# Kernel tuning notes

Measured on AMD Instinct MI355X. Metric: run time of the kernel, lower is better.

The kernel has to match this reference:

```python
import jax, jax.numpy as jnp
import numpy as np

B, H, P, L = 8, 512, 512, 2048
HIGH_STAB, LOW_STAB = 0.9, 0.99  # 0 <= high < |lambda| <= low <= 1 (discrete dynamics)


def setup_inputs() -> dict:
    key = jax.random.key(0)
    k_u, k_mag, k_ph, k_b, k_c, k_d = jax.random.split(key, 6)
    u = jax.random.normal(k_u, (B, H, L), dtype=jnp.float32)
    # Frozen diagonal reservoir state matrix Lambda_bar: complex eigenvalues with
    # magnitude in (high_stability, low_stability], random phase (stored as real/imag pairs).
    mag = jax.random.uniform(k_mag, (P,), minval=HIGH_STAB, maxval=LOW_STAB)
    phase = jax.random.uniform(k_ph, (P,), minval=0.0, maxval=2.0 * np.pi)
    Lambda_bar_ri = jnp.stack([mag * jnp.cos(phase), mag * jnp.sin(phase)], axis=-1)  # (P,2)
    B_bar_ri = jax.random.normal(k_b, (P, H, 2), dtype=jnp.float32)  # complex B_bar as real pairs
    C_ri = jax.random.normal(k_c, (H, P, 2), dtype=jnp.float32)      # complex C as real pairs
    D = jax.random.normal(k_d, (H, H), dtype=jnp.float32)
    return {"u": u, "Lambda_bar_ri": Lambda_bar_ri, "B_bar_ri": B_bar_ri, "C_ri": C_ri, "D": D}


def _binary_op(e_i, e_j):
    A_i, Bu_i = e_i
    A_j, Bu_j = e_j
    return (A_j * A_i, A_j * Bu_i + Bu_j)


def reference(u, Lambda_bar_ri, B_bar_ri, C_ri, D):
    Lam = jax.lax.complex(Lambda_bar_ri[:, 0], Lambda_bar_ri[:, 1])        # (P,)
    B_bar = jax.lax.complex(B_bar_ri[..., 0], B_bar_ri[..., 1])            # (P,H)
    C = jax.lax.complex(C_ri[..., 0], C_ri[..., 1])                        # (H,P)
    # Bu_t = B_bar @ u_t for all t, batched: (B,P,L) complex
    Bu = jnp.einsum('ph,bhl->bpl', B_bar, u.astype(B_bar.dtype))
    A = jnp.broadcast_to(Lam[None, :, None], Bu.shape)                     # (B,P,L)
    # Parallel associative scan: x_t = Lam * x_{t-1} + Bu_t
    _, x = jax.lax.associative_scan(_binary_op, (A, Bu), axis=2)           # (B,P,L)
    C_A_Bu = jnp.einsum('hp,bpl->bhl', C, x).real                          # (B,H,L)
    # torch.einsum('hh,bhl->bhl', D, u) uses only the diagonal of D
    Du = jnp.diagonal(D)[None, :, None] * u
    return jax.nn.gelu(C_A_Bu + Du, approximate=False)
```

## Files before the change

kernel.cpp:

```cpp
#include <hip/hip_runtime.h>
#include <cstdint>
#include <cstddef>

#define BB 8
#define HH 512
#define PP 512
#define LL 2048

typedef __attribute__((ext_vector_type(8))) __bf16 bf16x8;
typedef __attribute__((ext_vector_type(4))) float f32x4;

__device__ __forceinline__ uint16_t f2bf(float f) {
  uint32_t u = __builtin_bit_cast(uint32_t, f);
  u += 0x7FFFu + ((u >> 16) & 1u);
  return (uint16_t)(u >> 16);
}

__device__ __forceinline__ void async_copy16(const void* gptr, void* ldsptr) {
  __builtin_amdgcn_global_load_lds(
      (const __attribute__((address_space(1))) unsigned int*)gptr,
      (__attribute__((address_space(3))) unsigned int*)ldsptr,
      16, 0, 0);
}

__global__ __launch_bounds__(256) void prep_mats(
    const float* __restrict__ Bbar, const float* __restrict__ Cri,
    const float* __restrict__ Dm,
    uint16_t* __restrict__ A1, uint16_t* __restrict__ A2,
    float* __restrict__ Dd) {
  int idx = blockIdx.x * 256 + threadIdx.x;
  int p = idx >> 9, h = idx & 511;
  A1[(size_t)p * 512 + h]          = f2bf(Bbar[((size_t)p * 512 + h) * 2 + 0]);
  A1[(size_t)(512 + p) * 512 + h]  = f2bf(Bbar[((size_t)p * 512 + h) * 2 + 1]);
  int h2 = idx >> 9, p2 = idx & 511;
  A2[(size_t)h2 * 1024 + p2]        = f2bf( Cri[((size_t)h2 * 512 + p2) * 2 + 0]);
  A2[(size_t)h2 * 1024 + 512 + p2]  = f2bf(-Cri[((size_t)h2 * 512 + p2) * 2 + 1]);
  if (idx < 512) Dd[idx] = Dm[(size_t)idx * 512 + idx];
}

__global__ __launch_bounds__(256) void transpose_u_kernel(
    const float* __restrict__ U, uint16_t* __restrict__ Ut) {
  __shared__ __align__(16) uint16_t lds[64 * 72];
  const int t = threadIdx.x;
  const int b = blockIdx.z;
  const int l0 = blockIdx.x * 64, h0 = blockIdx.y * 64;
#pragma unroll
  for (int it = 0; it < 4; ++it) {
    int q = t + it * 256;
    int r = q >> 4;
    int c4 = q & 15;
    float4 v = *(const float4*)(U + ((size_t)(b * 512 + h0 + r)) * 2048 + l0 + c4 * 4);
    lds[(c4 * 4 + 0) * 72 + r] = f2bf(v.x);
    lds[(c4 * 4 + 1) * 72 + r] = f2bf(v.y);
    lds[(c4 * 4 + 2) * 72 + r] = f2bf(v.z);
    lds[(c4 * 4 + 3) * 72 + r] = f2bf(v.w);
  }
  __syncthreads();
#pragma unroll
  for (int it = 0; it < 2; ++it) {
    int q = t + it * 256;
    int r2 = q >> 3;
    int c8 = q & 7;
    uint4 w = *(const uint4*)&lds[r2 * 72 + c8 * 8];
    *(uint4*)(Ut + ((size_t)(b * 2048 + l0 + r2)) * 512 + h0 + c8 * 8) = w;
  }
}

__global__ __launch_bounds__(256) void transpose_x_kernel(
    const uint16_t* __restrict__ X, uint16_t* __restrict__ Xt) {
  __shared__ __align__(16) uint16_t lds[64 * 72];
  const int t = threadIdx.x;
  const int b = blockIdx.z;
  const int l0 = blockIdx.x * 64, k0 = blockIdx.y * 64;
#pragma unroll
  for (int it = 0; it < 2; ++it) {
    int q = t + it * 256;
    int r = q >> 3;
    int c8 = q & 7;
    uint4 v = *(const uint4*)(X + ((size_t)(b * 1024 + k0 + r)) * 2048 + l0 + c8 * 8);
    uint32_t wv[4] = {v.x, v.y, v.z, v.w};
#pragma unroll
    for (int d = 0; d < 4; ++d) {
      lds[(c8 * 8 + d * 2 + 0) * 72 + r] = (uint16_t)(wv[d] & 0xFFFFu);
      lds[(c8 * 8 + d * 2 + 1) * 72 + r] = (uint16_t)(wv[d] >> 16);
    }
  }
  __syncthreads();
#pragma unroll
  for (int it = 0; it < 2; ++it) {
    int q = t + it * 256;
    int r2 = q >> 3;
    int c8 = q & 7;
    uint4 w = *(const uint4*)&lds[r2 * 72 + c8 * 8];
    *(uint4*)(Xt + ((size_t)(b * 2048 + l0 + r2)) * 1024 + k0 + c8 * 8) = w;
  }
}

__global__ __launch_bounds__(256) void scan_kernel(
    const float* __restrict__ Lam, uint16_t* __restrict__ Bu) {
  const int gt = blockIdx.x * 256 + threadIdx.x;
  const int wave = gt >> 6, lane = gt & 63;
  const int b = wave >> 9, p = wave & 511;
  const float lr = Lam[p * 2 + 0], li = Lam[p * 2 + 1];
  float ar = lr, ai = li;
#pragma unroll
  for (int s = 0; s < 5; ++s) { float nr = ar * ar - ai * ai, ni = 2.f * ar * ai; ar = nr; ai = ni; }

  uint16_t* rowre = Bu + ((size_t)(b * 1024 + p)) * 2048 + lane * 32;
  uint16_t* rowim = Bu + ((size_t)(b * 1024 + 512 + p)) * 2048 + lane * 32;
  uint4 vr[4], vi[4];
#pragma unroll
  for (int q = 0; q < 4; ++q) { vr[q] = ((const uint4*)rowre)[q]; vi[q] = ((const uint4*)rowim)[q]; }

  float xr[32], xi[32];
  float sr = 0.f, si = 0.f;
#pragma unroll
  for (int q = 0; q < 4; ++q) {
    uint32_t wr[4] = {vr[q].x, vr[q].y, vr[q].z, vr[q].w};
    uint32_t wi[4] = {vi[q].x, vi[q].y, vi[q].z, vi[q].w};
#pragma unroll
    for (int d = 0; d < 4; ++d) {
      float br0 = __builtin_bit_cast(float, wr[d] << 16);
      float bi0 = __builtin_bit_cast(float, wi[d] << 16);
      float br1 = __builtin_bit_cast(float, wr[d] & 0xFFFF0000u);
      float bi1 = __builtin_bit_cast(float, wi[d] & 0xFFFF0000u);
      int j = q * 8 + d * 2;
      float nr = lr * sr - li * si + br0, ni = lr * si + li * sr + bi0;
      sr = nr; si = ni; xr[j] = sr; xi[j] = si;
      nr = lr * sr - li * si + br1; ni = lr * si + li * sr + bi1;
      sr = nr; si = ni; xr[j + 1] = sr; xi[j + 1] = si;
    }
  }
  float Ar = ar, Ai = ai, Sr = sr, Si = si;
#pragma unroll
  for (int off = 1; off < 64; off <<= 1) {
    float pAr = __shfl_up(Ar, off), pAi = __shfl_up(Ai, off);
    float pSr = __shfl_up(Sr, off), pSi = __shfl_up(Si, off);
    if (lane >= off) {
      float tSr = Ar * pSr - Ai * pSi + Sr;
      float tSi = Ar * pSi + Ai * pSr + Si;
      float tAr = Ar * pAr - Ai * pAi;
      float tAi = Ar * pAi + Ai * pAr;
      Sr = tSr; Si = tSi; Ar = tAr; Ai = tAi;
    }
  }
  float Cr = __shfl_up(Sr, 1), Ci = __shfl_up(Si, 1);
  if (lane == 0) { Cr = 0.f; Ci = 0.f; }
  float fr_ = lr * Cr - li * Ci, fi_ = lr * Ci + li * Cr;
#pragma unroll
  for (int j = 0; j < 32; ++j) {
    xr[j] += fr_; xi[j] += fi_;
    float nfr = fr_ * lr - fi_ * li, nfi = fr_ * li + fi_ * lr;
    fr_ = nfr; fi_ = nfi;
  }
#pragma unroll
  for (int q = 0; q < 4; ++q) {
    uint32_t wr[4], wi[4];
#pragma unroll
    for (int d = 0; d < 4; ++d) {
      int j = q * 8 + d * 2;
      wr[d] = (uint32_t)f2bf(xr[j]) | ((uint32_t)f2bf(xr[j + 1]) << 16);
      wi[d] = (uint32_t)f2bf(xi[j]) | ((uint32_t)f2bf(xi[j + 1]) << 16);
    }
    ((uint4*)rowre)[q] = make_uint4(wr[0], wr[1], wr[2], wr[3]);
    ((uint4*)rowim)[q] = make_uint4(wi[0], wi[1], wi[2], wi[3]);
  }
}

template <int K, bool EPI2>
__global__ __launch_bounds__(256) void gemm_kernel(
    const uint16_t* __restrict__ A, const uint16_t* __restrict__ Bt,
    uint16_t* __restrict__ Obf, float* __restrict__ Of32,
    const float* __restrict__ Dd, const float* __restrict__ Uu) {
  __shared__ __align__(16) uint16_t Alds[128 * 32];
  __shared__ __align__(16) uint16_t Blds[128 * 32];
  const int t = threadIdx.x, lane = t & 63, w = t >> 6;
  const int m0 = blockIdx.y * 128, n0 = blockIdx.x * 128, b = blockIdx.z;

  const int ra = t >> 2;
  const int ca = (t & 3) * 8;
  const uint16_t* gA0 = A + (size_t)(m0 + ra) * K + ca;
  const uint16_t* gA1 = A + (size_t)(m0 + 64 + ra) * K + ca;
  const uint16_t* gB0 = Bt + ((size_t)b * 2048 + n0 + ra) * K + ca;
  const uint16_t* gB1 = Bt + ((size_t)b * 2048 + n0 + 64 + ra) * K + ca;

  f32x4 acc[4][4];
#pragma unroll
  for (int i = 0; i < 4; ++i)
#pragma unroll
    for (int j = 0; j < 4; ++j) acc[i][j] = (f32x4){0.f, 0.f, 0.f, 0.f};

  const int wm = (w >> 1) * 64, wn = (w & 1) * 64;
  const int fr = lane & 15, fq = lane >> 4;

  for (int kb = 0; kb < K; kb += 32) {
    async_copy16(gA0 + kb, Alds + t * 8);
    async_copy16(gA1 + kb, Alds + 2048 + t * 8);
    async_copy16(gB0 + kb, Blds + t * 8);
    async_copy16(gB1 + kb, Blds + 2048 + t * 8);
    __syncthreads();
    bf16x8 af[4], bfr[4];
#pragma unroll
    for (int i = 0; i < 4; ++i) {
      af[i]  = *(const bf16x8*)&Alds[(wm + i * 16 + fr) * 32 + fq * 8];
      bfr[i] = *(const bf16x8*)&Blds[(wn + i * 16 + fr) * 32 + fq * 8];
    }
#pragma unroll
    for (int i = 0; i < 4; ++i)
#pragma unroll
      for (int j = 0; j < 4; ++j)
        acc[i][j] = __builtin_amdgcn_mfma_f32_16x16x32_bf16(af[i], bfr[j], acc[i][j], 0, 0, 0);
    __syncthreads();
  }

  if constexpr (!EPI2) {
    uint16_t* O = Obf + ((size_t)b * 1024 + m0) * 2048 + n0;
#pragma unroll
    for (int i = 0; i < 4; ++i)
#pragma unroll
      for (int j = 0; j < 4; ++j)
#pragma unroll
        for (int r = 0; r < 4; ++r) {
          int mm = wm + i * 16 + fq * 4 + r;
          int nn = wn + j * 16 + fr;
          O[(size_t)mm * 2048 + nn] = f2bf(acc[i][j][r]);
        }
  } else {
    const size_t base = ((size_t)b * 512 + m0) * 2048 + n0;
    float* O = Of32 + base;
    const float* Ub = Uu + base;
#pragma unroll
    for (int i = 0; i < 4; ++i)
#pragma unroll
      for (int r = 0; r < 4; ++r) {
        int mm = wm + i * 16 + fq * 4 + r;
        float dv = Dd[m0 + mm];
#pragma unroll
        for (int j = 0; j < 4; ++j) {
          int nn = wn + j * 16 + fr;
          float xv = acc[i][j][r] + dv * Ub[(size_t)mm * 2048 + nn];
          O[(size_t)mm * 2048 + nn] = 0.5f * xv * (1.f + erff(xv * 0.70710678118654752f));
        }
      }
  }
}

extern "C" void kernel_launch(void* const* d_in, const int* in_sizes, int n_in,
                              void* d_out, int out_size, void* d_ws, size_t ws_size,
                              hipStream_t stream) {
  const float* u    = (const float*)d_in[0];
  const float* Lam  = (const float*)d_in[1];
  const float* Bbar = (const float*)d_in[2];
  const float* Cri  = (const float*)d_in[3];
  const float* Dm   = (const float*)d_in[4];
  float* out = (float*)d_out;

  char* ws = (char*)d_ws;
  uint16_t* Bu  = (uint16_t*)(ws);
  uint16_t* u_t = (uint16_t*)(ws + 33554432);
  uint16_t* x_t = (uint16_t*)(ws + 33554432);
  uint16_t* A1  = (uint16_t*)(ws + 67108864);
  uint16_t* A2  = (uint16_t*)(ws + 68157440);
  float*    Dd  = (float*)   (ws + 69206016);

  prep_mats<<<1024, 256, 0, stream>>>(Bbar, Cri, Dm, A1, A2, Dd);
  transpose_u_kernel<<<dim3(32, 8, BB), 256, 0, stream>>>(u, u_t);
  gemm_kernel<512, false><<<dim3(16, 8, BB), 256, 0, stream>>>(A1, u_t, Bu, nullptr, nullptr, nullptr);
  scan_kernel<<<1024, 256, 0, stream>>>(Lam, Bu);
  transpose_x_kernel<<<dim3(32, 16, BB), 256, 0, stream>>>(Bu, x_t);
  gemm_kernel<1024, true><<<dim3(16, 4, BB), 256, 0, stream>>>(A2, x_t, nullptr, out, Dd, u);
}
```

Measured before the change: 193.5 us.

## Fuse u and x transposes into GEMM B-tile loads with swizzled LDS

Removes the two standalone transpose kernels. Each GEMM now reads its B operand in its original L-contiguous layout from global memory, converting to bf16 where needed, and transposes it while writing into LDS. XOR swizzles are added on both the A and B LDS tiles to reduce bank conflicts. This saves the workspace round-trips and two kernel launches. The cost is that B loads become synchronous register loads instead of async global-to-LDS copies, with extra ALU work inside the main loop.

```diff
diff --git a/kernel.cpp b/kernel.cpp
--- a/kernel.cpp
+++ b/kernel.cpp
@@ -38,64 +38,6 @@
   if (idx < 512) Dd[idx] = Dm[(size_t)idx * 512 + idx];
 }
 
-__global__ __launch_bounds__(256) void transpose_u_kernel(
-    const float* __restrict__ U, uint16_t* __restrict__ Ut) {
-  __shared__ __align__(16) uint16_t lds[64 * 72];
-  const int t = threadIdx.x;
-  const int b = blockIdx.z;
-  const int l0 = blockIdx.x * 64, h0 = blockIdx.y * 64;
-#pragma unroll
-  for (int it = 0; it < 4; ++it) {
-    int q = t + it * 256;
-    int r = q >> 4;
-    int c4 = q & 15;
-    float4 v = *(const float4*)(U + ((size_t)(b * 512 + h0 + r)) * 2048 + l0 + c4 * 4);
-    lds[(c4 * 4 + 0) * 72 + r] = f2bf(v.x);
-    lds[(c4 * 4 + 1) * 72 + r] = f2bf(v.y);
-    lds[(c4 * 4 + 2) * 72 + r] = f2bf(v.z);
-    lds[(c4 * 4 + 3) * 72 + r] = f2bf(v.w);
-  }
-  __syncthreads();
-#pragma unroll
-  for (int it = 0; it < 2; ++it) {
-    int q = t + it * 256;
-    int r2 = q >> 3;
-    int c8 = q & 7;
-    uint4 w = *(const uint4*)&lds[r2 * 72 + c8 * 8];
-    *(uint4*)(Ut + ((size_t)(b * 2048 + l0 + r2)) * 512 + h0 + c8 * 8) = w;
-  }
-}
-
-__global__ __launch_bounds__(256) void transpose_x_kernel(
-    const uint16_t* __restrict__ X, uint16_t* __restrict__ Xt) {
-  __shared__ __align__(16) uint16_t lds[64 * 72];
-  const int t = threadIdx.x;
-  const int b = blockIdx.z;
-  const int l0 = blockIdx.x * 64, k0 = blockIdx.y * 64;
-#pragma unroll
-  for (int it = 0; it < 2; ++it) {
-    int q = t + it * 256;
-    int r = q >> 3;
-    int c8 = q & 7;
-    uint4 v = *(const uint4*)(X + ((size_t)(b * 1024 + k0 + r)) * 2048 + l0 + c8 * 8);
-    uint32_t wv[4] = {v.x, v.y, v.z, v.w};
-#pragma unroll
-    for (int d = 0; d < 4; ++d) {
-      lds[(c8 * 8 + d * 2 + 0) * 72 + r] = (uint16_t)(wv[d] & 0xFFFFu);
-      lds[(c8 * 8 + d * 2 + 1) * 72 + r] = (uint16_t)(wv[d] >> 16);
-    }
-  }
-  __syncthreads();
-#pragma unroll
-  for (int it = 0; it < 2; ++it) {
-    int q = t + it * 256;
-    int r2 = q >> 3;
-    int c8 = q & 7;
-    uint4 w = *(const uint4*)&lds[r2 * 72 + c8 * 8];
-    *(uint4*)(Xt + ((size_t)(b * 2048 + l0 + r2)) * 1024 + k0 + c8 * 8) = w;
-  }
-}
-
 __global__ __launch_bounds__(256) void scan_kernel(
     const float* __restrict__ Lam, uint16_t* __restrict__ Bu) {
   const int gt = blockIdx.x * 256 + threadIdx.x;
@@ -167,22 +109,22 @@
   }
 }
 
-template <int K, bool EPI2>
-__global__ __launch_bounds__(256) void gemm_kernel(
-    const uint16_t* __restrict__ A, const uint16_t* __restrict__ Bt,
-    uint16_t* __restrict__ Obf, float* __restrict__ Of32,
-    const float* __restrict__ Dd, const float* __restrict__ Uu) {
+__global__ __launch_bounds__(256) void gemm1_fused(
+    const uint16_t* __restrict__ A, const float* __restrict__ U,
+    uint16_t* __restrict__ Bu) {
   __shared__ __align__(16) uint16_t Alds[128 * 32];
-  __shared__ __align__(16) uint16_t Blds[128 * 32];
+  __shared__ __align__(16) uint16_t Blds[128 * 40];
   const int t = threadIdx.x, lane = t & 63, w = t >> 6;
   const int m0 = blockIdx.y * 128, n0 = blockIdx.x * 128, b = blockIdx.z;
 
   const int ra = t >> 2;
-  const int ca = (t & 3) * 8;
-  const uint16_t* gA0 = A + (size_t)(m0 + ra) * K + ca;
-  const uint16_t* gA1 = A + (size_t)(m0 + 64 + ra) * K + ca;
-  const uint16_t* gB0 = Bt + ((size_t)b * 2048 + n0 + ra) * K + ca;
-  const uint16_t* gB1 = Bt + ((size_t)b * 2048 + n0 + 64 + ra) * K + ca;
+  const int qa = ((t & 3) ^ ((ra >> 1) & 3)) * 8;
+  const uint16_t* gA0 = A + (size_t)(m0 + ra) * 512 + qa;
+  const uint16_t* gA1 = A + (size_t)(m0 + 64 + ra) * 512 + qa;
+
+  const int kp = t >> 4, lg = t & 15;
+  const float* gB = U + ((size_t)b * 512 + 2 * kp) * 2048 + n0 + lg * 8;
+  const int bcol = ((kp >> 2) ^ (lg & 3)) * 8 + (kp & 3) * 2;
 
   f32x4 acc[4][4];
 #pragma unroll
@@ -192,18 +134,32 @@
 
   const int wm = (w >> 1) * 64, wn = (w & 1) * 64;
   const int fr = lane & 15, fq = lane >> 4;
-
-  for (int kb = 0; kb < K; kb += 32) {
-    async_copy16(gA0 + kb, Alds + t * 8);
-    async_copy16(gA1 + kb, Alds + 2048 + t * 8);
-    async_copy16(gB0 + kb, Blds + t * 8);
-    async_copy16(gB1 + kb, Blds + 2048 + t * 8);
+  const int aswz = (fq ^ ((fr >> 1) & 3)) * 8;
+
+  for (int kb = 0; kb < 512; kb += 32) {
+    async_copy16(gA0 + kb, Alds + (size_t)t * 8);
+    async_copy16(gA1 + kb, Alds + 2048 + (size_t)t * 8);
+    const float* s0 = gB + (size_t)kb * 2048;
+    float4 a0 = *(const float4*)(s0);
+    float4 a1 = *(const float4*)(s0 + 4);
+    float4 b0 = *(const float4*)(s0 + 2048);
+    float4 b1 = *(const float4*)(s0 + 2052);
+    float r0[8] = {a0.x, a0.y, a0.z, a0.w, a1.x, a1.y, a1.z, a1.w};
+    float r1[8] = {b0.x, b0.y, b0.z, b0.w, b1.x, b1.y, b1.z, b1.w};
+#pragma unroll
+    for (int j = 0; j < 8; ++j) {
+      uint32_t wv = (uint32_t)f2bf(r0[j]) | ((uint32_t)f2bf(r1[j]) << 16);
+      *(uint32_t*)&Blds[(lg * 8 + j) * 40 + bcol] = wv;
+    }
     __syncthreads();
     bf16x8 af[4], bfr[4];
 #pragma unroll
-    for (int i = 0; i < 4; ++i) {
-      af[i]  = *(const bf16x8*)&Alds[(wm + i * 16 + fr) * 32 + fq * 8];
-      bfr[i] = *(const bf16x8*)&Blds[(wn + i * 16 + fr) * 32 + fq * 8];
+    for (int i = 0; i < 4; ++i)
+      af[i] = *(const bf16x8*)&Alds[(wm + i * 16 + fr) * 32 + aswz];
+#pragma unroll
+    for (int j = 0; j < 4; ++j) {
+      int n = wn + j * 16 + fr;
+      bfr[j] = *(const bf16x8*)&Blds[n * 40 + ((fq ^ ((n >> 3) & 3)) * 8)];
     }
 #pragma unroll
     for (int i = 0; i < 4; ++i)
@@ -213,36 +169,96 @@
     __syncthreads();
   }
 
-  if constexpr (!EPI2) {
-    uint16_t* O = Obf + ((size_t)b * 1024 + m0) * 2048 + n0;
-#pragma unroll
-    for (int i = 0; i < 4; ++i)
-#pragma unroll
-      for (int j = 0; j < 4; ++j)
-#pragma unroll
-        for (int r = 0; r < 4; ++r) {
-          int mm = wm + i * 16 + fq * 4 + r;
-          int nn = wn + j * 16 + fr;
-          O[(size_t)mm * 2048 + nn] = f2bf(acc[i][j][r]);
-        }
-  } else {
-    const size_t base = ((size_t)b * 512 + m0) * 2048 + n0;
-    float* O = Of32 + base;
-    const float* Ub = Uu + base;
-#pragma unroll
-    for (int i = 0; i < 4; ++i)
+  uint16_t* O = Bu + ((size_t)b * 1024 + m0) * 2048 + n0;
+#pragma unroll
+  for (int i = 0; i < 4; ++i)
+#pragma unroll
+    for (int j = 0; j < 4; ++j)
 #pragma unroll
       for (int r = 0; r < 4; ++r) {
         int mm = wm + i * 16 + fq * 4 + r;
-        float dv = Dd[m0 + mm];
-#pragma unroll
-        for (int j = 0; j < 4; ++j) {
-          int nn = wn + j * 16 + fr;
-          float xv = acc[i][j][r] + dv * Ub[(size_t)mm * 2048 + nn];
-          O[(size_t)mm * 2048 + nn] = 0.5f * xv * (1.f + erff(xv * 0.70710678118654752f));
-        }
+        int nn = wn + j * 16 + fr;
+        O[(size_t)mm * 2048 + nn] = f2bf(acc[i][j][r]);
       }
-  }
+}
+
+__global__ __launch_bounds__(256) void gemm2_fused(
+    const uint16_t* __restrict__ A, const uint16_t* __restrict__ X,
+    float* __restrict__ Out, const float* __restrict__ Dd,
+    const float* __restrict__ Uu) {
+  __shared__ __align__(16) uint16_t Alds[128 * 32];
+  __shared__ __align__(16) uint16_t Blds[128 * 40];
+  const int t = threadIdx.x, lane = t & 63, w = t >> 6;
+  const int m0 = blockIdx.y * 128, n0 = blockIdx.x * 128, b = blockIdx.z;
+
+  const int ra = t >> 2;
+  const int qa = ((t & 3) ^ ((ra >> 1) & 3)) * 8;
+  const uint16_t* gA0 = A + (size_t)(m0 + ra) * 1024 + qa;
+  const uint16_t* gA1 = A + (size_t)(m0 + 64 + ra) * 1024 + qa;
+
+  const int kp = t >> 4, lg = t & 15;
+  const uint16_t* gB = X + ((size_t)b * 1024 + 2 * kp) * 2048 + n0 + lg * 8;
+  const int bcol = ((kp >> 2) ^ (lg & 3)) * 8 + (kp & 3) * 2;
+
+  f32x4 acc[4][4];
+#pragma unroll
+  for (int i = 0; i < 4; ++i)
+#pragma unroll
+    for (int j = 0; j < 4; ++j) acc[i][j] = (f32x4){0.f, 0.f, 0.f, 0.f};
+
+  const int wm = (w >> 1) * 64, wn = (w & 1) * 64;
+  const int fr = lane & 15, fq = lane >> 4;
+  const int aswz = (fq ^ ((fr >> 1) & 3)) * 8;
+
+  for (int kb = 0; kb < 1024; kb += 32) {
+    async_copy16(gA0 + kb, Alds + (size_t)t * 8);
+    async_copy16(gA1 + kb, Alds + 2048 + (size_t)t * 8);
+    const uint16_t* s0 = gB + (size_t)kb * 2048;
+    uint4 q0 = *(const uint4*)(s0);
+    uint4 q1 = *(const uint4*)(s0 + 2048);
+    uint32_t u0[4] = {q0.x, q0.y, q0.z, q0.w};
+    uint32_t u1[4] = {q1.x, q1.y, q1.z, q1.w};
+#pragma unroll
+    for (int d = 0; d < 4; ++d) {
+      uint32_t lo = (u0[d] & 0xFFFFu) | (u1[d] << 16);
+      uint32_t hi = (u0[d] >> 16) | (u1[d] & 0xFFFF0000u);
+      *(uint32_t*)&Blds[(lg * 8 + 2 * d + 0) * 40 + bcol] = lo;
+      *(uint32_t*)&Blds[(lg * 8 + 2 * d + 1) * 40 + bcol] = hi;
+    }
+    __syncthreads();
+    bf16x8 af[4], bfr[4];
+#pragma unroll
+    for (int i = 0; i < 4; ++i)
+      af[i] = *(const bf16x8*)&Alds[(wm + i * 16 + fr) * 32 + aswz];
+#pragma unroll
+    for (int j = 0; j < 4; ++j) {
+      int n = wn + j * 16 + fr;
+      bfr[j] = *(const bf16x8*)&Blds[n * 40 + ((fq ^ ((n >> 3) & 3)) * 8)];
+    }
+#pragma unroll
+    for (int i = 0; i < 4; ++i)
+#pragma unroll
+      for (int j = 0; j < 4; ++j)
+        acc[i][j] = __builtin_amdgcn_mfma_f32_16x16x32_bf16(af[i], bfr[j], acc[i][j], 0, 0, 0);
+    __syncthreads();
+  }
+
+  const size_t base = ((size_t)b * 512 + m0) * 2048 + n0;
+  float* O = Out + base;
+  const float* Ub = Uu + base;
+#pragma unroll
+  for (int i = 0; i < 4; ++i)
+#pragma unroll
+    for (int r = 0; r < 4; ++r) {
+      int mm = wm + i * 16 + fq * 4 + r;
+      float dv = Dd[m0 + mm];
+#pragma unroll
+      for (int j = 0; j < 4; ++j) {
+        int nn = wn + j * 16 + fr;
+        float xv = acc[i][j][r] + dv * Ub[(size_t)mm * 2048 + nn];
+        O[(size_t)mm * 2048 + nn] = 0.5f * xv * (1.f + erff(xv * 0.70710678118654752f));
+      }
+    }
 }
 
 extern "C" void kernel_launch(void* const* d_in, const int* in_sizes, int n_in,
@@ -256,17 +272,13 @@
   float* out = (float*)d_out;
 
   char* ws = (char*)d_ws;
-  uint16_t* Bu  = (uint16_t*)(ws);
-  uint16_t* u_t = (uint16_t*)(ws + 33554432);
-  uint16_t* x_t = (uint16_t*)(ws + 33554432);
-  uint16_t* A1  = (uint16_t*)(ws + 67108864);
-  uint16_t* A2  = (uint16_t*)(ws + 68157440);
-  float*    Dd  = (float*)   (ws + 69206016);
+  uint16_t* Bu = (uint16_t*)(ws);
+  uint16_t* A1 = (uint16_t*)(ws + 33554432);
+  uint16_t* A2 = (uint16_t*)(ws + 34603008);
+  float*    Dd = (float*)   (ws + 35651584);
 
   prep_mats<<<1024, 256, 0, stream>>>(Bbar, Cri, Dm, A1, A2, Dd);
-  transpose_u_kernel<<<dim3(32, 8, BB), 256, 0, stream>>>(u, u_t);
-  gemm_kernel<512, false><<<dim3(16, 8, BB), 256, 0, stream>>>(A1, u_t, Bu, nullptr, nullptr, nullptr);
+  gemm1_fused<<<dim3(16, 8, BB), 256, 0, stream>>>(A1, u, Bu);
   scan_kernel<<<1024, 256, 0, stream>>>(Lam, Bu);
-  transpose_x_kernel<<<dim3(32, 16, BB), 256, 0, stream>>>(Bu, x_t);
-  gemm_kernel<1024, true><<<dim3(16, 4, BB), 256, 0, stream>>>(A2, x_t, nullptr, out, Dd, u);
-}
+  gemm2_fused<<<dim3(16, 4, BB), 256, 0, stream>>>(A2, Bu, out, Dd, u);
+}
```

After: 199.8 us. 1.03x slower.
